# Kernel tuning notes

Measured on AMD Instinct MI355X. Metric: run time of the kernel, lower is better.

## Reference

```python
import jax, jax.numpy as jnp
import numpy as np

N = 50000
E = 600000
IN_DIM = 256
OUT_DIM = 128
SCALE = 1.8
K = 2
ALPHA = 0.15
EPS = 1e-12  # matches F.normalize eps


def setup_inputs() -> dict:
    key = jax.random.key(0)
    k1, k2, k3, k4 = jax.random.split(key, 4)
    x = jax.random.normal(k1, (N, IN_DIM), dtype=jnp.float32)
    edge_index = jax.random.randint(k2, (2, E), 0, N, dtype=jnp.int64)
    # nn.Linear params (Kaiming-uniform-ish init scale)
    lim = 1.0 / np.sqrt(IN_DIM)
    W = jax.random.uniform(k3, (OUT_DIM, IN_DIM), dtype=jnp.float32, minval=-lim, maxval=lim)
    b = jax.random.uniform(k4, (OUT_DIM,), dtype=jnp.float32, minval=-lim, maxval=lim)
    return {"x": x, "edge_index": edge_index, "W": W, "b": b}


def _gcn_norm(edge_index, num_nodes):
    # add self loops, symmetric normalization D^-1/2 A D^-1/2
    loops = jnp.arange(num_nodes, dtype=edge_index.dtype)
    row = jnp.concatenate([edge_index[0], loops])  # source
    col = jnp.concatenate([edge_index[1], loops])  # target
    deg = jax.ops.segment_sum(jnp.ones_like(col, dtype=jnp.float32), col,
                              num_segments=num_nodes)
    dinv = jnp.where(deg > 0, jax.lax.rsqrt(deg), 0.0)
    w = dinv[row] * dinv[col]
    return row, col, w


def reference(x, edge_index, W, b):
    # linear
    h = x @ W.T + b  # [N, OUT_DIM]
    # L2 normalize over feature dim, then scale
    nrm = jnp.sqrt(jnp.sum(h * h, axis=1, keepdims=True))
    h = h / jnp.maximum(nrm, EPS) * SCALE
    # APPNP propagation (eval mode: edge dropout disabled)
    row, col, w = _gcn_norm(edge_index, N)
    z = h
    for _ in range(K):
        msg = w[:, None] * z[row]  # gather + weight, [E+N, OUT_DIM]
        agg = jax.ops.segment_sum(msg, col, num_segments=N)
        z = (1.0 - ALPHA) * agg + ALPHA * h
    return z
```

## Files before the change

### kernel.cpp

```cpp
#include <hip/hip_runtime.h>
#include <hip/hip_bf16.h>

#define NNODES 50000
#define IN_DIM 256
#define OUT_DIM 128
#define SCALE 1.8f
#define ALPHA 0.15f
#define NB_SCAN 196

typedef unsigned short ushort_t;
typedef __attribute__((ext_vector_type(8))) _Float16 f16x8;
typedef __attribute__((ext_vector_type(4))) float f32x4;


__device__ __forceinline__ unsigned short f2bf_rne(float f) {
    unsigned int u = __float_as_uint(f);
    unsigned int r = u + 0x7fffu + ((u >> 16) & 1u);
    return (unsigned short)(r >> 16);
}

__device__ __forceinline__ float2 bf2_to_f2(unsigned int p) {
    float2 f;
    f.x = __uint_as_float(p << 16);
    f.y = __uint_as_float(p & 0xffff0000u);
    return f;
}

__device__ __forceinline__ unsigned int f2_to_bf2(float x, float y) {
    return (unsigned int)f2bf_rne(x) | ((unsigned int)f2bf_rne(y) << 16);
}

__device__ __forceinline__ unsigned short f2h(float f) {
    _Float16 h = (_Float16)f;
    return *(unsigned short*)&h;
}


__global__ void deg_scatter_kernel(const int* __restrict__ col, int* __restrict__ cnt, int E) {
    int e = blockIdx.x * blockDim.x + threadIdx.x;
    if (e < E) atomicAdd(&cnt[col[e]], 1);
}


__global__ void wcvt_kernel(const float* __restrict__ W, ushort_t* __restrict__ Whf) {
    int i = blockIdx.x * blockDim.x + threadIdx.x;
    if (i < OUT_DIM * IN_DIM) Whf[i] = f2h(W[i]);
}


__global__ void scan_pass1(const int* __restrict__ cnt, int* __restrict__ part) {
    __shared__ int sd[256];
    int t = threadIdx.x;
    int i = blockIdx.x * 256 + t;
    sd[t] = (i < NNODES) ? cnt[i] : 0;
    __syncthreads();
    for (int s = 128; s > 0; s >>= 1) {
        if (t < s) sd[t] += sd[t + s];
        __syncthreads();
    }
    if (t == 0) part[blockIdx.x] = sd[0];
}

__global__ void scan_pass2(int* __restrict__ part) {
    __shared__ int s[256];
    int t = threadIdx.x;
    int v = (t < NB_SCAN) ? part[t] : 0;
    s[t] = v;
    __syncthreads();
    for (int o = 1; o < 256; o <<= 1) {
        int u = (t >= o) ? s[t - o] : 0;
        __syncthreads();
        s[t] += u;
        __syncthreads();
    }
    if (t < NB_SCAN) part[t] = (t == 0) ? 0 : s[t - 1];
}

__global__ void scan_pass3(const int* __restrict__ cnt, const int* __restrict__ part,
                           int* __restrict__ off, int* __restrict__ cur,
                           float* __restrict__ dinv, float* __restrict__ selfw, int E) {
    __shared__ int s[256];
    int t = threadIdx.x;
    int i = blockIdx.x * 256 + t;
    int v = (i < NNODES) ? cnt[i] : 0;
    s[t] = v;
    __syncthreads();
    for (int o = 1; o < 256; o <<= 1) {
        int u = (t >= o) ? s[t - o] : 0;
        __syncthreads();
        s[t] += u;
        __syncthreads();
    }
    int excl = part[blockIdx.x] + ((t == 0) ? 0 : s[t - 1]);
    if (i < NNODES) {
        off[i] = excl;
        cur[i] = excl;
        float d = rsqrtf((float)(v + 1));
        dinv[i] = d;
        selfw[i] = (1.0f - ALPHA) * d * d;
    }
    if (i == NNODES - 1) off[NNODES] = E;
}

__global__ void csr_fill_kernel(const int* __restrict__ row, const int* __restrict__ col,
                                const float* __restrict__ dinv, int* __restrict__ cur,
                                int* __restrict__ csr_row, float* __restrict__ csr_w, int E) {
    int e = blockIdx.x * blockDim.x + threadIdx.x;
    if (e < E) {
        int c = col[e];
        int r = row[e];
        int p = atomicAdd(&cur[c], 1);
        csr_row[p] = r;
        csr_w[p] = (1.0f - ALPHA) * dinv[r] * dinv[c];
    }
}


#define XPAD 264

__global__ void __launch_bounds__(256, 4) gemm_norm_kernel(
        const float* __restrict__ x, const ushort_t* __restrict__ Whf,
        const float* __restrict__ b, ushort_t* __restrict__ zb) {
    __shared__ __align__(16) ushort_t xh[64][XPAD];

    const int t = threadIdx.x;
    const int wv = t >> 6;
    const int lane = t & 63;
    const int q = lane >> 4;
    const int c = lane & 15;
    const int rowBase = blockIdx.x * 64;

    f16x8 wf[2][8];
    float bias[2];
    #pragma unroll
    for (int j = 0; j < 2; ++j) {
        const size_t base = (size_t)((2 * wv + j) * 16 + c) * IN_DIM + q * 8;
        #pragma unroll
        for (int kt = 0; kt < 8; ++kt)
            wf[j][kt] = *(const f16x8*)(Whf + base + kt * 32);
        bias[j] = b[(2 * wv + j) * 16 + c];
    }

    #pragma unroll
    for (int it = 0; it < 16; ++it) {
        int s = it * 256 + t;
        int r = s >> 6;
        int ks = (s & 63) * 4;
        int grow = rowBase + r;
        float4 v = make_float4(0.f, 0.f, 0.f, 0.f);
        if (grow < NNODES) v = *(const float4*)(x + (size_t)grow * IN_DIM + ks);
        uint2 p;
        p.x = (unsigned int)f2h(v.x) | ((unsigned int)f2h(v.y) << 16);
        p.y = (unsigned int)f2h(v.z) | ((unsigned int)f2h(v.w) << 16);
        *(uint2*)&xh[r][ks] = p;
    }
    __syncthreads();

    f32x4 acc[4][2];
    #pragma unroll
    for (int m = 0; m < 4; ++m)
        #pragma unroll
        for (int j = 0; j < 2; ++j) {
            acc[m][j][0] = bias[j]; acc[m][j][1] = bias[j];
            acc[m][j][2] = bias[j]; acc[m][j][3] = bias[j];
        }

    #pragma unroll
    for (int kt = 0; kt < 8; ++kt) {
        const int kb = kt * 32 + q * 8;
        #pragma unroll
        for (int m = 0; m < 4; ++m) {
            f16x8 a = *(const f16x8*)&xh[m * 16 + c][kb];
            #pragma unroll
            for (int j = 0; j < 2; ++j)
                acc[m][j] = __builtin_amdgcn_mfma_f32_16x16x32_f16(a, wf[j][kt], acc[m][j], 0, 0, 0);
        }
    }

    float psum[4][4];
    #pragma unroll
    for (int m = 0; m < 4; ++m)
        #pragma unroll
        for (int r = 0; r < 4; ++r)
            psum[m][r] = acc[m][0][r] * acc[m][0][r] + acc[m][1][r] * acc[m][1][r];
    #pragma unroll
    for (int mask = 1; mask < 16; mask <<= 1)
        #pragma unroll
        for (int m = 0; m < 4; ++m)
            #pragma unroll
            for (int r = 0; r < 4; ++r)
                psum[m][r] += __shfl_xor(psum[m][r], mask);

    __syncthreads();
    float* red = (float*)&xh[0][0];
    float* scl = red + 64 * 8;
    if (c == 0) {
        #pragma unroll
        for (int m = 0; m < 4; ++m)
            #pragma unroll
            for (int r = 0; r < 4; ++r)
                red[(m * 16 + q * 4 + r) * 8 + wv] = psum[m][r];
    }
    __syncthreads();
    if (t < 64) {
        float s = red[t * 8 + 0] + red[t * 8 + 1] + red[t * 8 + 2] + red[t * 8 + 3];
        scl[t] = SCALE / fmaxf(sqrtf(s), 1e-12f);
    }
    __syncthreads();

    #pragma unroll
    for (int m = 0; m < 4; ++m) {
        #pragma unroll
        for (int r = 0; r < 4; ++r) {
            int lrow = m * 16 + q * 4 + r;
            int grow = rowBase + lrow;
            if (grow < NNODES) {
                float sc = scl[lrow];
                #pragma unroll
                for (int j = 0; j < 2; ++j) {
                    float o = acc[m][j][r] * sc;
                    zb[(size_t)grow * OUT_DIM + (2 * wv + j) * 16 + c] = f2bf_rne(o);
                }
            }
        }
    }
}


template <int FINAL>
__global__ void __launch_bounds__(256) gather_kernel(
        const int* __restrict__ off, const int* __restrict__ csr_row,
        const float* __restrict__ csr_w, const float* __restrict__ selfw,
        const unsigned int* __restrict__ zst, const unsigned int* __restrict__ hb,
        unsigned int* __restrict__ zout_b, float* __restrict__ zout_f) {
    const int wv = threadIdx.x >> 6;
    const int lane = threadIdx.x & 63;
    const int c = blockIdx.x * 4 + wv;
    const int s = off[c];
    const int e = off[c + 1];

    float2 acc;
    {
        float sw = selfw[c] + (FINAL ? 0.0f : ALPHA);
        float2 zc = bf2_to_f2(zst[(size_t)c * 64 + lane]);
        acc.x = sw * zc.x;
        acc.y = sw * zc.y;
    }

    for (int base = s; base < e; base += 64) {
        int n = e - base;
        if (n > 64) n = 64;
        int idx = 0;
        float w = 0.f;
        if (lane < n) {
            idx = csr_row[base + lane];
            w = csr_w[base + lane];
        }
        int j = 0;
        for (; j + 4 <= n; j += 4) {
            int r0 = __shfl(idx, j + 0), r1 = __shfl(idx, j + 1);
            int r2 = __shfl(idx, j + 2), r3 = __shfl(idx, j + 3);
            float w0 = __shfl(w, j + 0), w1 = __shfl(w, j + 1);
            float w2 = __shfl(w, j + 2), w3 = __shfl(w, j + 3);
            unsigned int p0 = zst[(size_t)r0 * 64 + lane];
            unsigned int p1 = zst[(size_t)r1 * 64 + lane];
            unsigned int p2 = zst[(size_t)r2 * 64 + lane];
            unsigned int p3 = zst[(size_t)r3 * 64 + lane];
            float2 v0 = bf2_to_f2(p0), v1 = bf2_to_f2(p1);
            float2 v2 = bf2_to_f2(p2), v3 = bf2_to_f2(p3);
            acc.x += w0 * v0.x; acc.y += w0 * v0.y;
            acc.x += w1 * v1.x; acc.y += w1 * v1.y;
            acc.x += w2 * v2.x; acc.y += w2 * v2.y;
            acc.x += w3 * v3.x; acc.y += w3 * v3.y;
        }
        for (; j < n; ++j) {
            int r = __shfl(idx, j);
            float ww = __shfl(w, j);
            float2 v = bf2_to_f2(zst[(size_t)r * 64 + lane]);
            acc.x += ww * v.x;
            acc.y += ww * v.y;
        }
    }

    if (FINAL) {
        float2 h = bf2_to_f2(hb[(size_t)c * 64 + lane]);
        float ox = acc.x + ALPHA * h.x;
        float oy = acc.y + ALPHA * h.y;
        ((float2*)zout_f)[(size_t)c * 64 + lane] = make_float2(ox, oy);
    } else {
        zout_b[(size_t)c * 64 + lane] = f2_to_bf2(acc.x, acc.y);
    }
}

extern "C" void kernel_launch(void* const* d_in, const int* in_sizes, int n_in,
                              void* d_out, int out_size, void* d_ws, size_t ws_size,
                              hipStream_t stream) {
    const float* x  = (const float*)d_in[0];
    const int*   ei = (const int*)d_in[1];
    const float* W  = (const float*)d_in[2];
    const float* b  = (const float*)d_in[3];
    float* out = (float*)d_out;

    int E = in_sizes[1] / 2;
    const int* row = ei;
    const int* col = ei + E;

    float* dinv  = (float*)d_ws;
    float* selfw = dinv + 50048;
    unsigned int* zb  = (unsigned int*)(selfw + 50048);
    unsigned int* z1b = zb + (size_t)NNODES * 64;
    int*   cnt   = (int*)(z1b + (size_t)NNODES * 64);
    int*   off   = cnt + 50048;
    int*   cur   = off + 50112;
    int*   part  = cur + 50048;
    int*   csr_row = part + 256;
    float* csr_w   = (float*)(csr_row + ((E + 63) & ~63));
    ushort_t* Whf  = (ushort_t*)(csr_w + ((E + 63) & ~63));

    hipMemsetAsync(cnt, 0, NNODES * sizeof(int), stream);
    deg_scatter_kernel<<<(E + 255) / 256, 256, 0, stream>>>(col, cnt, E);
    wcvt_kernel<<<(OUT_DIM * IN_DIM + 255) / 256, 256, 0, stream>>>(W, Whf);

    scan_pass1<<<NB_SCAN, 256, 0, stream>>>(cnt, part);
    scan_pass2<<<1, 256, 0, stream>>>(part);
    scan_pass3<<<NB_SCAN, 256, 0, stream>>>(cnt, part, off, cur, dinv, selfw, E);
    csr_fill_kernel<<<(E + 255) / 256, 256, 0, stream>>>(row, col, dinv, cur, csr_row, csr_w, E);

    gemm_norm_kernel<<<(NNODES + 63) / 64, 256, 0, stream>>>(x, Whf, b, (ushort_t*)zb);

    gather_kernel<0><<<NNODES / 4, 256, 0, stream>>>(off, csr_row, csr_w, selfw, zb, nullptr, z1b, nullptr);
    gather_kernel<1><<<NNODES / 4, 256, 0, stream>>>(off, csr_row, csr_w, selfw, z1b, zb, nullptr, out);
}
```

Baseline: 245.2 us.

## Prescale features by D^-1/2 to drop per-edge weights from propagation

Stores features pre-multiplied by the inverse-sqrt degree, so neighbour aggregation becomes an unweighted sum followed by a per-node scale. This removes the per-edge weight array, its construction in CSR fill, and its loads and shuffles in both gather passes. The final pass recovers the unscaled residual through a per-node sqrt(deg) factor. Storing the scaled values in bf16 slightly changes rounding behaviour.

```diff
diff --git a/kernel.cpp b/kernel.cpp
--- a/kernel.cpp
+++ b/kernel.cpp
@@ -78,7 +78,8 @@
 
 __global__ void scan_pass3(const int* __restrict__ cnt, const int* __restrict__ part,
                            int* __restrict__ off, int* __restrict__ cur,
-                           float* __restrict__ dinv, float* __restrict__ selfw, int E) {
+                           float* __restrict__ dinv, float* __restrict__ q,
+                           float2* __restrict__ gr, int E) {
     __shared__ int s[256];
     int t = threadIdx.x;
     int i = blockIdx.x * 256 + t;
@@ -95,23 +96,22 @@
     if (i < NNODES) {
         off[i] = excl;
         cur[i] = excl;
-        float d = rsqrtf((float)(v + 1));
+        float deg = (float)(v + 1);
+        float d = rsqrtf(deg);
         dinv[i] = d;
-        selfw[i] = (1.0f - ALPHA) * d * d;
+        q[i] = (1.0f - ALPHA) * d * d;
+        gr[i] = make_float2((1.0f - ALPHA) * d, ALPHA * sqrtf(deg));
     }
     if (i == NNODES - 1) off[NNODES] = E;
 }
 
 __global__ void csr_fill_kernel(const int* __restrict__ row, const int* __restrict__ col,
-                                const float* __restrict__ dinv, int* __restrict__ cur,
-                                int* __restrict__ csr_row, float* __restrict__ csr_w, int E) {
+                                int* __restrict__ cur, int* __restrict__ csr_row, int E) {
     int e = blockIdx.x * blockDim.x + threadIdx.x;
     if (e < E) {
         int c = col[e];
-        int r = row[e];
         int p = atomicAdd(&cur[c], 1);
-        csr_row[p] = r;
-        csr_w[p] = (1.0f - ALPHA) * dinv[r] * dinv[c];
+        csr_row[p] = row[e];
     }
 }
 
@@ -120,7 +120,8 @@
 
 __global__ void __launch_bounds__(256, 4) gemm_norm_kernel(
         const float* __restrict__ x, const ushort_t* __restrict__ Whf,
-        const float* __restrict__ b, ushort_t* __restrict__ zb) {
+        const float* __restrict__ b, const float* __restrict__ dinv,
+        ushort_t* __restrict__ s0b) {
     __shared__ __align__(16) ushort_t xh[64][XPAD];
 
     const int t = threadIdx.x;
@@ -204,7 +205,7 @@
     __syncthreads();
     if (t < 64) {
         float s = red[t * 8 + 0] + red[t * 8 + 1] + red[t * 8 + 2] + red[t * 8 + 3];
-        scl[t] = SCALE / fmaxf(sqrtf(s), 1e-12f);
+        scl[t] = dinv[rowBase + t] * SCALE / fmaxf(sqrtf(s), 1e-12f);
     }
     __syncthreads();
 
@@ -219,7 +220,7 @@
                 #pragma unroll
                 for (int j = 0; j < 2; ++j) {
                     float o = acc[m][j][r] * sc;
-                    zb[(size_t)grow * OUT_DIM + (2 * wv + j) * 16 + c] = f2bf_rne(o);
+                    s0b[(size_t)grow * OUT_DIM + (2 * wv + j) * 16 + c] = f2bf_rne(o);
                 }
             }
         }
@@ -230,9 +231,9 @@
 template <int FINAL>
 __global__ void __launch_bounds__(256) gather_kernel(
         const int* __restrict__ off, const int* __restrict__ csr_row,
-        const float* __restrict__ csr_w, const float* __restrict__ selfw,
-        const unsigned int* __restrict__ zst, const unsigned int* __restrict__ hb,
-        unsigned int* __restrict__ zout_b, float* __restrict__ zout_f) {
+        const float* __restrict__ q, const float2* __restrict__ gr,
+        const unsigned int* __restrict__ sin, const unsigned int* __restrict__ s0,
+        unsigned int* __restrict__ sout_b, float* __restrict__ out_f) {
     const int wv = threadIdx.x >> 6;
     const int lane = threadIdx.x & 63;
     const int c = blockIdx.x * 4 + wv;
@@ -240,55 +241,49 @@
     const int e = off[c + 1];
 
     float2 acc;
+    float2 zc0;
     {
-        float sw = selfw[c] + (FINAL ? 0.0f : ALPHA);
-        float2 zc = bf2_to_f2(zst[(size_t)c * 64 + lane]);
-        acc.x = sw * zc.x;
-        acc.y = sw * zc.y;
+        float2 zc = bf2_to_f2(sin[(size_t)c * 64 + lane]);
+        acc = zc;
+        zc0 = FINAL ? bf2_to_f2(s0[(size_t)c * 64 + lane]) : zc;
     }
 
     for (int base = s; base < e; base += 64) {
         int n = e - base;
         if (n > 64) n = 64;
         int idx = 0;
-        float w = 0.f;
-        if (lane < n) {
-            idx = csr_row[base + lane];
-            w = csr_w[base + lane];
-        }
+        if (lane < n) idx = csr_row[base + lane];
         int j = 0;
         for (; j + 4 <= n; j += 4) {
             int r0 = __shfl(idx, j + 0), r1 = __shfl(idx, j + 1);
             int r2 = __shfl(idx, j + 2), r3 = __shfl(idx, j + 3);
-            float w0 = __shfl(w, j + 0), w1 = __shfl(w, j + 1);
-            float w2 = __shfl(w, j + 2), w3 = __shfl(w, j + 3);
-            unsigned int p0 = zst[(size_t)r0 * 64 + lane];
-            unsigned int p1 = zst[(size_t)r1 * 64 + lane];
-            unsigned int p2 = zst[(size_t)r2 * 64 + lane];
-            unsigned int p3 = zst[(size_t)r3 * 64 + lane];
+            unsigned int p0 = sin[(size_t)r0 * 64 + lane];
+            unsigned int p1 = sin[(size_t)r1 * 64 + lane];
+            unsigned int p2 = sin[(size_t)r2 * 64 + lane];
+            unsigned int p3 = sin[(size_t)r3 * 64 + lane];
             float2 v0 = bf2_to_f2(p0), v1 = bf2_to_f2(p1);
             float2 v2 = bf2_to_f2(p2), v3 = bf2_to_f2(p3);
-            acc.x += w0 * v0.x; acc.y += w0 * v0.y;
-            acc.x += w1 * v1.x; acc.y += w1 * v1.y;
-            acc.x += w2 * v2.x; acc.y += w2 * v2.y;
-            acc.x += w3 * v3.x; acc.y += w3 * v3.y;
+            acc.x += v0.x + v1.x + v2.x + v3.x;
+            acc.y += v0.y + v1.y + v2.y + v3.y;
         }
         for (; j < n; ++j) {
             int r = __shfl(idx, j);
-            float ww = __shfl(w, j);
-            float2 v = bf2_to_f2(zst[(size_t)r * 64 + lane]);
-            acc.x += ww * v.x;
-            acc.y += ww * v.y;
+            float2 v = bf2_to_f2(sin[(size_t)r * 64 + lane]);
+            acc.x += v.x;
+            acc.y += v.y;
         }
     }
 
     if (FINAL) {
-        float2 h = bf2_to_f2(hb[(size_t)c * 64 + lane]);
-        float ox = acc.x + ALPHA * h.x;
-        float oy = acc.y + ALPHA * h.y;
-        ((float2*)zout_f)[(size_t)c * 64 + lane] = make_float2(ox, oy);
+        float2 g = gr[c];
+        float ox = g.x * acc.x + g.y * zc0.x;
+        float oy = g.x * acc.y + g.y * zc0.y;
+        ((float2*)out_f)[(size_t)c * 64 + lane] = make_float2(ox, oy);
     } else {
-        zout_b[(size_t)c * 64 + lane] = f2_to_bf2(acc.x, acc.y);
+        float qc = q[c];
+        float ox = qc * acc.x + ALPHA * zc0.x;
+        float oy = qc * acc.y + ALPHA * zc0.y;
+        sout_b[(size_t)c * 64 + lane] = f2_to_bf2(ox, oy);
     }
 }
 
@@ -305,17 +300,17 @@
     const int* row = ei;
     const int* col = ei + E;
 
-    float* dinv  = (float*)d_ws;
-    float* selfw = dinv + 50048;
-    unsigned int* zb  = (unsigned int*)(selfw + 50048);
-    unsigned int* z1b = zb + (size_t)NNODES * 64;
-    int*   cnt   = (int*)(z1b + (size_t)NNODES * 64);
+    float*  dinv = (float*)d_ws;
+    float*  q    = dinv + 50048;
+    float2* gr   = (float2*)(q + 50048);
+    unsigned int* s0b = (unsigned int*)(gr + 50048);
+    unsigned int* s1b = s0b + (size_t)NNODES * 64;
+    int*   cnt   = (int*)(s1b + (size_t)NNODES * 64);
     int*   off   = cnt + 50048;
     int*   cur   = off + 50112;
     int*   part  = cur + 50048;
     int*   csr_row = part + 256;
-    float* csr_w   = (float*)(csr_row + ((E + 63) & ~63));
-    ushort_t* Whf  = (ushort_t*)(csr_w + ((E + 63) & ~63));
+    ushort_t* Whf  = (ushort_t*)(csr_row + ((E + 63) & ~63));
 
     hipMemsetAsync(cnt, 0, NNODES * sizeof(int), stream);
     deg_scatter_kernel<<<(E + 255) / 256, 256, 0, stream>>>(col, cnt, E);
@@ -323,11 +318,11 @@
 
     scan_pass1<<<NB_SCAN, 256, 0, stream>>>(cnt, part);
     scan_pass2<<<1, 256, 0, stream>>>(part);
-    scan_pass3<<<NB_SCAN, 256, 0, stream>>>(cnt, part, off, cur, dinv, selfw, E);
-    csr_fill_kernel<<<(E + 255) / 256, 256, 0, stream>>>(row, col, dinv, cur, csr_row, csr_w, E);
-
-    gemm_norm_kernel<<<(NNODES + 63) / 64, 256, 0, stream>>>(x, Whf, b, (ushort_t*)zb);
-
-    gather_kernel<0><<<NNODES / 4, 256, 0, stream>>>(off, csr_row, csr_w, selfw, zb, nullptr, z1b, nullptr);
-    gather_kernel<1><<<NNODES / 4, 256, 0, stream>>>(off, csr_row, csr_w, selfw, z1b, zb, nullptr, out);
-}
+    scan_pass3<<<NB_SCAN, 256, 0, stream>>>(cnt, part, off, cur, dinv, q, gr, E);
+    csr_fill_kernel<<<(E + 255) / 256, 256, 0, stream>>>(row, col, cur, csr_row, E);
+
+    gemm_norm_kernel<<<(NNODES + 63) / 64, 256, 0, stream>>>(x, Whf, b, dinv, (ushort_t*)s0b);
+
+    gather_kernel<0><<<NNODES / 4, 256, 0, stream>>>(off, csr_row, q, gr, s0b, s0b, s1b, nullptr);
+    gather_kernel<1><<<NNODES / 4, 256, 0, stream>>>(off, csr_row, q, gr, s1b, s0b, nullptr, out);
+}
```

Result: faster. 234.2 us (-4.5%).
